# Kernel tuning notes

Measured on AMD Instinct MI355X. Metric: run time of the kernel, lower is better.

## Reference

```python
import jax, jax.numpy as jnp
import numpy as np

D_MODEL = 512
NUM_HEADS = 8


def setup_inputs() -> dict:
    key = jax.random.key(0)
    ks = jax.random.split(key, 12)
    B, S, D = 2, 4096, D_MODEL
    s = 1.0 / np.sqrt(D)
    return {
        "q": jax.random.normal(ks[0], (B, S, D), jnp.float32),
        "k": jax.random.normal(ks[1], (B, S, D), jnp.float32),
        "v": jax.random.normal(ks[2], (B, S, D), jnp.float32),
        "w_q": jax.random.normal(ks[3], (D, D), jnp.float32) * s,
        "b_q": jax.random.normal(ks[4], (D,), jnp.float32) * s,
        "w_k": jax.random.normal(ks[5], (D, D), jnp.float32) * s,
        "b_k": jax.random.normal(ks[6], (D,), jnp.float32) * s,
        "w_v": jax.random.normal(ks[7], (D, D), jnp.float32) * s,
        "b_v": jax.random.normal(ks[8], (D,), jnp.float32) * s,
        "w_o": jax.random.normal(ks[9], (D, D), jnp.float32) * s,
        "b_o": jax.random.normal(ks[10], (D,), jnp.float32) * s,
    }


def _split(x, num_heads):
    B, S, D = x.shape
    return x.reshape(B, S, num_heads, D // num_heads).transpose(0, 2, 1, 3)


def reference(q, k, v, w_q, b_q, w_k, b_k, w_v, b_v, w_o, b_o):
    # Linear projections (torch Linear: x @ W^T + b)
    qp = q @ w_q.T + b_q
    kp = k @ w_k.T + b_k
    vp = v @ w_v.T + b_v
    # split into heads: [B, H, S, d_head]
    qh = _split(qp, NUM_HEADS)
    kh = _split(kp, NUM_HEADS)
    vh = _split(vp, NUM_HEADS)
    d_head = qh.shape[-1]
    # NOTE: original scales by sqrt(d_model of the per-head tensor) == sqrt(d_head)
    score = jnp.einsum("bhqd,bhkd->bhqk", qh, kh) / jnp.sqrt(jnp.float32(d_head))
    attn = jax.nn.softmax(score, axis=-1)  # full [B,H,S,S] materialized, as in source
    out = jnp.einsum("bhqk,bhkd->bhqd", attn, vh)
    # concat heads back to [B, S, D]
    B, H, S, Dh = out.shape
    out = out.transpose(0, 2, 1, 3).reshape(B, S, H * Dh)
    return out @ w_o.T + b_o
```

## Files before the change

### kernel.cpp

```cpp
#include <hip/hip_runtime.h>
#include <math.h>

typedef __bf16 bf16_t;
typedef __bf16 bf16x4_v __attribute__((ext_vector_type(4)));
typedef __bf16 bf16x8_t __attribute__((ext_vector_type(8)));
typedef float f32x4_t __attribute__((ext_vector_type(4)));
typedef short short4_t __attribute__((ext_vector_type(4)));
typedef unsigned uint2_t __attribute__((ext_vector_type(2)));

#define S_LEN 4096
#define DM 512
#define NH 8
#define DH 64
#define MTOT 8192

#define Q_SCALE 0.1803368801111204f

#define REG   4194304
#define WREG  262144
#define W_OFF (3 * REG)
#define CVT_TOTAL (3 * REG + 4 * WREG)
#define QH_OFF CVT_TOTAL

__device__ inline f32x4_t mfma16(bf16x8_t a, bf16x8_t b, f32x4_t c) {
    return __builtin_amdgcn_mfma_f32_16x16x32_bf16(a, b, c, 0, 0, 0);
}

__device__ inline f32x4_t mfma_pv(short4_t a, short4_t b, f32x4_t c) {
    return __builtin_amdgcn_mfma_f32_16x16x16bf16_1k(a, b, c, 0, 0, 0);
}

__device__ inline unsigned pkbf16(float a, float b) {
    unsigned short ra = __builtin_bit_cast(unsigned short, (bf16_t)a);
    unsigned short rb = __builtin_bit_cast(unsigned short, (bf16_t)b);
    return (unsigned)ra | ((unsigned)rb << 16);
}

__device__ inline void async_copy16(const void* g, void* l) {
    __builtin_amdgcn_global_load_lds(
        (const __attribute__((address_space(1))) void*)g,
        (__attribute__((address_space(3))) void*)l, 16, 0, 0);
}

__global__ __launch_bounds__(256) void cvt_all(
    const float* __restrict__ q, const float* __restrict__ k, const float* __restrict__ v,
    const float* __restrict__ wq, const float* __restrict__ wk,
    const float* __restrict__ wv, const float* __restrict__ wo,
    bf16_t* __restrict__ dst)
{
    long gidx = (long)blockIdx.x * 2048 + (long)threadIdx.x * 8;
    const float* src;
    long off = gidx;
    if      (gidx < 1L * REG)          { src = q; }
    else if (gidx < 2L * REG)          { src = k;  off = gidx - 1L * REG; }
    else if (gidx < 3L * REG)          { src = v;  off = gidx - 2L * REG; }
    else if (gidx < W_OFF + 1L * WREG) { src = wq; off = gidx - W_OFF; }
    else if (gidx < W_OFF + 2L * WREG) { src = wk; off = gidx - (W_OFF + 1L * WREG); }
    else if (gidx < W_OFF + 3L * WREG) { src = wv; off = gidx - (W_OFF + 2L * WREG); }
    else                               { src = wo; off = gidx - (W_OFF + 3L * WREG); }
    float4 a = *(const float4*)(src + off);
    float4 b = *(const float4*)(src + off + 4);
    bf16x8_t h;
    h[0] = (bf16_t)a.x; h[1] = (bf16_t)a.y; h[2] = (bf16_t)a.z; h[3] = (bf16_t)a.w;
    h[4] = (bf16_t)b.x; h[5] = (bf16_t)b.y; h[6] = (bf16_t)b.z; h[7] = (bf16_t)b.w;
    *(bf16x8_t*)(dst + gidx) = h;
}

__global__ __launch_bounds__(256) void gemm_qkv(
    const bf16_t* __restrict__ XWb,
    const float* __restrict__ B0, const float* __restrict__ B1, const float* __restrict__ B2,
    bf16_t* __restrict__ dst_base)
{
    const int p = blockIdx.z;
    const bf16_t* __restrict__ X = XWb + (size_t)p * REG;
    const bf16_t* __restrict__ W = XWb + W_OFF + (size_t)p * WREG;
    const float* __restrict__ Bi = (p == 0) ? B0 : ((p == 1) ? B1 : B2);
    bf16_t* __restrict__ dst = dst_base + (size_t)p * REG;

    const int m0 = blockIdx.x * 128;
    const int n0 = blockIdx.y * 128;
    const int tid = threadIdx.x;
    const int lane = tid & 63, wid = tid >> 6;
    const int lm = lane & 15, lg = lane >> 4;
    const int wm = (wid >> 1) * 64, wn = (wid & 1) * 64;

    __shared__ __align__(16) bf16_t As[128 * 64];
    __shared__ __align__(16) bf16_t Bs[128 * 64];

    f32x4_t acc[4][4] = {};

    const int r0 = tid >> 3, c7 = tid & 7;
    const int cA0 = ((lg) ^ (lm & 7)) * 8;
    const int cA1 = ((4 + lg) ^ (lm & 7)) * 8;

    for (int kb = 0; kb < DM / 64; ++kb) {
        const int k0 = kb * 64;
#pragma unroll
        for (int i = 0; i < 4; ++i) {
            int row = i * 32 + r0;
            int ch = c7 ^ (row & 7);
            async_copy16(X + (size_t)(m0 + row) * DM + k0 + ch * 8, (char*)As + (i * 256 + tid) * 16);
            async_copy16(W + (size_t)(n0 + row) * DM + k0 + ch * 8, (char*)Bs + (i * 256 + tid) * 16);
        }
        __syncthreads();
#pragma unroll
        for (int kd = 0; kd < 2; ++kd) {
            const int co = kd ? cA1 : cA0;
            bf16x8_t fa[4], fb[4];
#pragma unroll
            for (int mt = 0; mt < 4; ++mt) {
                fa[mt] = *(const bf16x8_t*)(As + (wm + mt * 16 + lm) * 64 + co);
                fb[mt] = *(const bf16x8_t*)(Bs + (wn + mt * 16 + lm) * 64 + co);
            }
            if (p < 2) {
#pragma unroll
                for (int mt = 0; mt < 4; ++mt)
#pragma unroll
                    for (int nt = 0; nt < 4; ++nt)
                        acc[nt][mt] = mfma16(fb[nt], fa[mt], acc[nt][mt]);
            } else {
#pragma unroll
                for (int mt = 0; mt < 4; ++mt)
#pragma unroll
                    for (int nt = 0; nt < 4; ++nt)
                        acc[mt][nt] = mfma16(fa[mt], fb[nt], acc[mt][nt]);
            }
        }
        __syncthreads();
    }

    if (p == 2) {
#pragma unroll
        for (int nt = 0; nt < 4; ++nt) {
            int col = n0 + wn + nt * 16 + lm;
            float bv = Bi[col];
            int h = (col >> 6) & 7, dc = col & 63;
#pragma unroll
            for (int mt = 0; mt < 4; ++mt) {
                int mrow = m0 + wm + mt * 16 + lg * 4;
                int bb = mrow >> 12, s = mrow & (S_LEN - 1);
                bf16x4_v pk;
#pragma unroll
                for (int r = 0; r < 4; ++r) pk[r] = (bf16_t)(acc[mt][nt][r] + bv);
                *(bf16x4_v*)&dst[(((size_t)(bb * NH + h)) * DH + dc) * S_LEN + s] = pk;
            }
        }
    } else {
        const float scale = (p == 0) ? Q_SCALE : 1.0f;
#pragma unroll
        for (int nt = 0; nt < 4; ++nt) {
            int ncol = n0 + wn + nt * 16 + lg * 4;
            float4 bv4 = *(const float4*)&Bi[ncol];
            int h = (ncol >> 6) & 7, dc = ncol & 63;
#pragma unroll
            for (int mt = 0; mt < 4; ++mt) {
                int m = m0 + wm + mt * 16 + lm;
                int bb = m >> 12, s = m & (S_LEN - 1);
                bf16x4_v pk;
                pk[0] = (bf16_t)((acc[nt][mt][0] + bv4.x) * scale);
                pk[1] = (bf16_t)((acc[nt][mt][1] + bv4.y) * scale);
                pk[2] = (bf16_t)((acc[nt][mt][2] + bv4.z) * scale);
                pk[3] = (bf16_t)((acc[nt][mt][3] + bv4.w) * scale);
                *(bf16x4_v*)&dst[(((size_t)(bb * NH + h)) * S_LEN + s) * DH + dc] = pk;
            }
        }
    }
}

__global__ __launch_bounds__(512, 4) void flash_attn(
    const bf16_t* __restrict__ Qh, const bf16_t* __restrict__ Kh,
    const bf16_t* __restrict__ Vth, bf16_t* __restrict__ O)
{
    const int bh = blockIdx.y;
    const int q0 = blockIdx.x * 128;
    const int tid = threadIdx.x;
    const int lane = tid & 63, wid = tid >> 6;
    const int lm = lane & 15, lg = lane >> 4;
    const int qg = wid & 3;
    const int kvh = wid >> 2;

    const bf16_t* __restrict__ Qb  = Qh  + (size_t)bh * S_LEN * DH;
    const bf16_t* __restrict__ Kb  = Kh  + (size_t)bh * S_LEN * DH;
    const bf16_t* __restrict__ Vtg = Vth + (size_t)bh * S_LEN * DH;

    __shared__ __align__(16) char smem[35328];

    bf16x8_t bQ[2][2];
#pragma unroll
    for (int nt = 0; nt < 2; ++nt)
#pragma unroll
        for (int kd = 0; kd < 2; ++kd)
            bQ[nt][kd] = *(const bf16x8_t*)(Qb + (size_t)(q0 + qg * 32 + nt * 16 + lm) * DH + kd * 32 + lg * 8);

    f32x4_t o_acc[4][2] = {};
    float l_acc[2] = {0.f, 0.f};

    const int srow = tid >> 3;
    const int slch = (tid & 7) ^ (srow & 7);
    char* lK0 = smem + tid * 16;
    char* lK1 = smem + 8192 + tid * 16;
    char* lV0 = smem + 16384 + tid * 16;
    char* lV1 = smem + 24576 + tid * 16;
    const bf16_t* gK = Kb + (size_t)srow * DH + slch * 8;
    const bf16_t* gV = Vtg + (size_t)srow * S_LEN + slch * 8;

    const int cK0 = ((lg) ^ (lm & 7)) * 16;
    const int cK1 = ((4 + lg) ^ (lm & 7)) * 16;
    const char* ksb = smem + kvh * 8192;
    const char* vsb = smem + 16384 + kvh * 8192;

    for (int it = 0; it < S_LEN / 128; ++it) {
        const int kvb = it * 128;
        async_copy16(gK + (size_t)kvb * DH, lK0);
        async_copy16(gK + (size_t)(kvb + 64) * DH, lK1);
        async_copy16(gV + kvb, lV0);
        async_copy16(gV + kvb + 64, lV1);
        __syncthreads();

        unsigned pk[4][2][2];
#pragma unroll
        for (int mt = 0; mt < 4; ++mt) {
            const char* krow = ksb + (mt * 16 + lm) * 128;
            bf16x8_t aK0 = *(const bf16x8_t*)(krow + cK0);
            bf16x8_t aK1 = *(const bf16x8_t*)(krow + cK1);
            f32x4_t s0 = {}, s1 = {};
            s0 = mfma16(aK0, bQ[0][0], s0);
            s0 = mfma16(aK1, bQ[0][1], s0);
            s1 = mfma16(aK0, bQ[1][0], s1);
            s1 = mfma16(aK1, bQ[1][1], s1);
            float e0 = __builtin_amdgcn_exp2f(s0[0]);
            float e1 = __builtin_amdgcn_exp2f(s0[1]);
            float e2 = __builtin_amdgcn_exp2f(s0[2]);
            float e3 = __builtin_amdgcn_exp2f(s0[3]);
            pk[mt][0][0] = pkbf16(e0, e1);
            pk[mt][0][1] = pkbf16(e2, e3);
            l_acc[0] += (e0 + e1) + (e2 + e3);
            float f0 = __builtin_amdgcn_exp2f(s1[0]);
            float f1 = __builtin_amdgcn_exp2f(s1[1]);
            float f2 = __builtin_amdgcn_exp2f(s1[2]);
            float f3 = __builtin_amdgcn_exp2f(s1[3]);
            pk[mt][1][0] = pkbf16(f0, f1);
            pk[mt][1][1] = pkbf16(f2, f3);
            l_acc[1] += (f0 + f1) + (f2 + f3);
        }

#pragma unroll
        for (int mt = 0; mt < 4; ++mt) {
            const char* vrow = vsb + (mt * 16 + lm) * 128;
#pragma unroll
            for (int c = 0; c < 4; ++c) {
                int pc = (c * 2 + (lg >> 1)) ^ (lm & 7);
                short4_t vA = *(const short4_t*)(vrow + pc * 16 + (lg & 1) * 8);
                short4_t bP0 = __builtin_bit_cast(short4_t, (uint2_t){pk[c][0][0], pk[c][0][1]});
                short4_t bP1 = __builtin_bit_cast(short4_t, (uint2_t){pk[c][1][0], pk[c][1][1]});
                o_acc[mt][0] = mfma_pv(vA, bP0, o_acc[mt][0]);
                o_acc[mt][1] = mfma_pv(vA, bP1, o_acc[mt][1]);
            }
        }
        __syncthreads();
    }

#pragma unroll
    for (int nt = 0; nt < 2; ++nt) {
        l_acc[nt] += __shfl_xor(l_acc[nt], 16, 64);
        l_acc[nt] += __shfl_xor(l_acc[nt], 32, 64);
    }

    float* ob = (float*)smem + qg * (32 * 66);
    float* lb = (float*)(smem + 33792);

    if (kvh == 1) {
#pragma unroll
        for (int nt = 0; nt < 2; ++nt) {
#pragma unroll
            for (int mt = 0; mt < 4; ++mt)
#pragma unroll
                for (int r = 0; r < 4; ++r)
                    ob[(nt * 16 + lm) * 66 + mt * 16 + lg * 4 + r] = o_acc[mt][nt][r];
            if (lg == 0) lb[qg * 32 + nt * 16 + lm] = l_acc[nt];
        }
    }
    __syncthreads();
    if (kvh == 0) {
        const int bb = bh >> 3, h = bh & 7;
#pragma unroll
        for (int nt = 0; nt < 2; ++nt) {
            float ltot = l_acc[nt] + lb[qg * 32 + nt * 16 + lm];
            float inv = 1.0f / ltot;
            int q = q0 + qg * 32 + nt * 16 + lm;
            size_t base = ((size_t)(bb * S_LEN + q)) * DM + h * DH;
#pragma unroll
            for (int mt = 0; mt < 4; ++mt) {
                const float* orow = &ob[(nt * 16 + lm) * 66 + mt * 16 + lg * 4];
                bf16x4_v pkd;
#pragma unroll
                for (int r = 0; r < 4; ++r)
                    pkd[r] = (bf16_t)((o_acc[mt][nt][r] + orow[r]) * inv);
                *(bf16x4_v*)&O[base + mt * 16 + lg * 4] = pkd;
            }
        }
    }
}

__global__ __launch_bounds__(256) void gemm_out(
    const bf16_t* __restrict__ A, const bf16_t* __restrict__ W,
    const float* __restrict__ Bi, float* __restrict__ out)
{
    const int m0 = blockIdx.x * 64;
    const int n0 = blockIdx.y * 128;
    const int tid = threadIdx.x;
    const int lane = tid & 63, wid = tid >> 6;
    const int lm = lane & 15, lg = lane >> 4;
    const int wm = (wid >> 1) * 32, wn = (wid & 1) * 64;

    __shared__ __align__(16) bf16_t As[64 * 64];
    __shared__ __align__(16) bf16_t Bs[128 * 64];

    f32x4_t acc[4][2] = {};

    const int r0 = tid >> 3, c7 = tid & 7;
    const int cA0 = ((lg) ^ (lm & 7)) * 8;
    const int cA1 = ((4 + lg) ^ (lm & 7)) * 8;

    for (int kb = 0; kb < DM / 64; ++kb) {
        const int k0 = kb * 64;
#pragma unroll
        for (int i = 0; i < 2; ++i) {
            int idx = i * 256 + tid;
            int row = idx >> 3;
            int ch = (idx & 7) ^ (row & 7);
            async_copy16(A + (size_t)(m0 + row) * DM + k0 + ch * 8, (char*)As + idx * 16);
        }
#pragma unroll
        for (int i = 0; i < 4; ++i) {
            int row = i * 32 + r0;
            int ch = c7 ^ (row & 7);
            async_copy16(W + (size_t)(n0 + row) * DM + k0 + ch * 8, (char*)Bs + (i * 256 + tid) * 16);
        }
        __syncthreads();
#pragma unroll
        for (int kd = 0; kd < 2; ++kd) {
            const int co = kd ? cA1 : cA0;
            bf16x8_t fa[2], fb[4];
#pragma unroll
            for (int mt = 0; mt < 2; ++mt)
                fa[mt] = *(const bf16x8_t*)(As + (wm + mt * 16 + lm) * 64 + co);
#pragma unroll
            for (int nt = 0; nt < 4; ++nt)
                fb[nt] = *(const bf16x8_t*)(Bs + (wn + nt * 16 + lm) * 64 + co);
#pragma unroll
            for (int nt = 0; nt < 4; ++nt)
#pragma unroll
                for (int mt = 0; mt < 2; ++mt)
                    acc[nt][mt] = mfma16(fb[nt], fa[mt], acc[nt][mt]);
        }
        __syncthreads();
    }

#pragma unroll
    for (int nt = 0; nt < 4; ++nt) {
        int ncol = n0 + wn + nt * 16 + lg * 4;
        float4 bv4 = *(const float4*)&Bi[ncol];
#pragma unroll
        for (int mt = 0; mt < 2; ++mt) {
            int m = m0 + wm + mt * 16 + lm;
            float4 ov;
            ov.x = acc[nt][mt][0] + bv4.x;
            ov.y = acc[nt][mt][1] + bv4.y;
            ov.z = acc[nt][mt][2] + bv4.z;
            ov.w = acc[nt][mt][3] + bv4.w;
            *(float4*)&out[(size_t)m * DM + ncol] = ov;
        }
    }
}

extern "C" void kernel_launch(void* const* d_in, const int* in_sizes, int n_in,
                              void* d_out, int out_size, void* d_ws, size_t ws_size,
                              hipStream_t stream)
{
    const float* q  = (const float*)d_in[0];
    const float* k  = (const float*)d_in[1];
    const float* v  = (const float*)d_in[2];
    const float* wq = (const float*)d_in[3];
    const float* bq = (const float*)d_in[4];
    const float* wk = (const float*)d_in[5];
    const float* bk = (const float*)d_in[6];
    const float* wv = (const float*)d_in[7];
    const float* bv = (const float*)d_in[8];
    const float* wo = (const float*)d_in[9];
    const float* bo = (const float*)d_in[10];
    float* out = (float*)d_out;

    bf16_t* ws = (bf16_t*)d_ws;
    bf16_t* XWb = ws;
    bf16_t* Qh  = ws + QH_OFF;
    bf16_t* Kh  = Qh + REG;
    bf16_t* VTh = Kh + REG;
    bf16_t* Ob  = ws;
    bf16_t* Wob = ws + W_OFF + 3 * (size_t)WREG;

    cvt_all<<<CVT_TOTAL / 2048, 256, 0, stream>>>(q, k, v, wq, wk, wv, wo, XWb);

    dim3 g1(MTOT / 128, DM / 128, 3);
    gemm_qkv<<<g1, 256, 0, stream>>>(XWb, bq, bk, bv, Qh);

    dim3 g2(S_LEN / 128, 2 * NH, 1);
    flash_attn<<<g2, 512, 0, stream>>>(Qh, Kh, VTh, Ob);

    dim3 g3(MTOT / 64, DM / 128, 1);
    gemm_out<<<g3, 256, 0, stream>>>(Ob, Wob, bo, out);
}
```

Baseline: 234.9 us.

## Register-prefetch GEMM tiles and use K=32 MFMA for P·V

Result: faster. 229.9 us (-2.1%).

```diff
diff --git a/kernel.cpp b/kernel.cpp
--- a/kernel.cpp
+++ b/kernel.cpp
@@ -5,8 +5,8 @@
 typedef __bf16 bf16x4_v __attribute__((ext_vector_type(4)));
 typedef __bf16 bf16x8_t __attribute__((ext_vector_type(8)));
 typedef float f32x4_t __attribute__((ext_vector_type(4)));
-typedef short short4_t __attribute__((ext_vector_type(4)));
 typedef unsigned uint2_t __attribute__((ext_vector_type(2)));
+typedef unsigned uint4_t __attribute__((ext_vector_type(4)));
 
 #define S_LEN 4096
 #define DM 512
@@ -24,10 +24,6 @@
 
 __device__ inline f32x4_t mfma16(bf16x8_t a, bf16x8_t b, f32x4_t c) {
     return __builtin_amdgcn_mfma_f32_16x16x32_bf16(a, b, c, 0, 0, 0);
-}
-
-__device__ inline f32x4_t mfma_pv(short4_t a, short4_t b, f32x4_t c) {
-    return __builtin_amdgcn_mfma_f32_16x16x16bf16_1k(a, b, c, 0, 0, 0);
 }
 
 __device__ inline unsigned pkbf16(float a, float b) {
@@ -93,16 +89,32 @@
     const int cA0 = ((lg) ^ (lm & 7)) * 8;
     const int cA1 = ((4 + lg) ^ (lm & 7)) * 8;
 
+    int rows[4], chs[4];
+#pragma unroll
+    for (int i = 0; i < 4; ++i) { rows[i] = i * 32 + r0; chs[i] = c7 ^ (rows[i] & 7); }
+
+    uint4_t pA[4], pB[4];
+#pragma unroll
+    for (int i = 0; i < 4; ++i) {
+        pA[i] = *(const uint4_t*)(X + (size_t)(m0 + rows[i]) * DM + chs[i] * 8);
+        pB[i] = *(const uint4_t*)(W + (size_t)(n0 + rows[i]) * DM + chs[i] * 8);
+    }
+#pragma unroll
+    for (int i = 0; i < 4; ++i) {
+        *(uint4_t*)((char*)As + (i * 256 + tid) * 16) = pA[i];
+        *(uint4_t*)((char*)Bs + (i * 256 + tid) * 16) = pB[i];
+    }
+    __syncthreads();
+
     for (int kb = 0; kb < DM / 64; ++kb) {
-        const int k0 = kb * 64;
-#pragma unroll
-        for (int i = 0; i < 4; ++i) {
-            int row = i * 32 + r0;
-            int ch = c7 ^ (row & 7);
-            async_copy16(X + (size_t)(m0 + row) * DM + k0 + ch * 8, (char*)As + (i * 256 + tid) * 16);
-            async_copy16(W + (size_t)(n0 + row) * DM + k0 + ch * 8, (char*)Bs + (i * 256 + tid) * 16);
-        }
-        __syncthreads();
+        if (kb < DM / 64 - 1) {
+            const int k1 = (kb + 1) * 64;
+#pragma unroll
+            for (int i = 0; i < 4; ++i) {
+                pA[i] = *(const uint4_t*)(X + (size_t)(m0 + rows[i]) * DM + k1 + chs[i] * 8);
+                pB[i] = *(const uint4_t*)(W + (size_t)(n0 + rows[i]) * DM + k1 + chs[i] * 8);
+            }
+        }
 #pragma unroll
         for (int kd = 0; kd < 2; ++kd) {
             const int co = kd ? cA1 : cA0;
@@ -126,7 +138,15 @@
                         acc[mt][nt] = mfma16(fa[mt], fb[nt], acc[mt][nt]);
             }
         }
-        __syncthreads();
+        if (kb < DM / 64 - 1) {
+            __syncthreads();
+#pragma unroll
+            for (int i = 0; i < 4; ++i) {
+                *(uint4_t*)((char*)As + (i * 256 + tid) * 16) = pA[i];
+                *(uint4_t*)((char*)Bs + (i * 256 + tid) * 16) = pB[i];
+            }
+            __syncthreads();
+        }
     }
 
     if (p == 2) {
@@ -248,13 +268,17 @@
         for (int mt = 0; mt < 4; ++mt) {
             const char* vrow = vsb + (mt * 16 + lm) * 128;
 #pragma unroll
-            for (int c = 0; c < 4; ++c) {
-                int pc = (c * 2 + (lg >> 1)) ^ (lm & 7);
-                short4_t vA = *(const short4_t*)(vrow + pc * 16 + (lg & 1) * 8);
-                short4_t bP0 = __builtin_bit_cast(short4_t, (uint2_t){pk[c][0][0], pk[c][0][1]});
-                short4_t bP1 = __builtin_bit_cast(short4_t, (uint2_t){pk[c][1][0], pk[c][1][1]});
-                o_acc[mt][0] = mfma_pv(vA, bP0, o_acc[mt][0]);
-                o_acc[mt][1] = mfma_pv(vA, bP1, o_acc[mt][1]);
+            for (int cc = 0; cc < 2; ++cc) {
+                const int ca = 2 * cc, cb = 2 * cc + 1;
+                int pc0 = (ca * 2 + (lg >> 1)) ^ (lm & 7);
+                int pc1 = (cb * 2 + (lg >> 1)) ^ (lm & 7);
+                uint2_t va0 = *(const uint2_t*)(vrow + pc0 * 16 + (lg & 1) * 8);
+                uint2_t va1 = *(const uint2_t*)(vrow + pc1 * 16 + (lg & 1) * 8);
+                bf16x8_t vA = __builtin_bit_cast(bf16x8_t, (uint4_t){va0[0], va0[1], va1[0], va1[1]});
+                bf16x8_t bP0 = __builtin_bit_cast(bf16x8_t, (uint4_t){pk[ca][0][0], pk[ca][0][1], pk[cb][0][0], pk[cb][0][1]});
+                bf16x8_t bP1 = __builtin_bit_cast(bf16x8_t, (uint4_t){pk[ca][1][0], pk[ca][1][1], pk[cb][1][0], pk[cb][1][1]});
+                o_acc[mt][0] = mfma16(vA, bP0, o_acc[mt][0]);
+                o_acc[mt][1] = mfma16(vA, bP1, o_acc[mt][1]);
             }
         }
         __syncthreads();
@@ -322,22 +346,34 @@
     const int cA0 = ((lg) ^ (lm & 7)) * 8;
     const int cA1 = ((4 + lg) ^ (lm & 7)) * 8;
 
+    int arow[2], ach[2], brow[4], bch[4];
+#pragma unroll
+    for (int i = 0; i < 2; ++i) {
+        int idx = i * 256 + tid;
+        arow[i] = idx >> 3; ach[i] = (idx & 7) ^ (arow[i] & 7);
+    }
+#pragma unroll
+    for (int i = 0; i < 4; ++i) { brow[i] = i * 32 + r0; bch[i] = c7 ^ (brow[i] & 7); }
+
+    uint4_t pA[2], pB[4];
+#pragma unroll
+    for (int i = 0; i < 2; ++i) pA[i] = *(const uint4_t*)(A + (size_t)(m0 + arow[i]) * DM + ach[i] * 8);
+#pragma unroll
+    for (int i = 0; i < 4; ++i) pB[i] = *(const uint4_t*)(W + (size_t)(n0 + brow[i]) * DM + bch[i] * 8);
+#pragma unroll
+    for (int i = 0; i < 2; ++i) *(uint4_t*)((char*)As + (i * 256 + tid) * 16) = pA[i];
+#pragma unroll
+    for (int i = 0; i < 4; ++i) *(uint4_t*)((char*)Bs + (i * 256 + tid) * 16) = pB[i];
+    __syncthreads();
+
     for (int kb = 0; kb < DM / 64; ++kb) {
-        const int k0 = kb * 64;
-#pragma unroll
-        for (int i = 0; i < 2; ++i) {
-            int idx = i * 256 + tid;
-            int row = idx >> 3;
-            int ch = (idx & 7) ^ (row & 7);
-            async_copy16(A + (size_t)(m0 + row) * DM + k0 + ch * 8, (char*)As + idx * 16);
-        }
-#pragma unroll
-        for (int i = 0; i < 4; ++i) {
-            int row = i * 32 + r0;
-            int ch = c7 ^ (row & 7);
-            async_copy16(W + (size_t)(n0 + row) * DM + k0 + ch * 8, (char*)Bs + (i * 256 + tid) * 16);
-        }
-        __syncthreads();
+        if (kb < DM / 64 - 1) {
+            const int k1 = (kb + 1) * 64;
+#pragma unroll
+            for (int i = 0; i < 2; ++i) pA[i] = *(const uint4_t*)(A + (size_t)(m0 + arow[i]) * DM + k1 + ach[i] * 8);
+#pragma unroll
+            for (int i = 0; i < 4; ++i) pB[i] = *(const uint4_t*)(W + (size_t)(n0 + brow[i]) * DM + k1 + bch[i] * 8);
+        }
 #pragma unroll
         for (int kd = 0; kd < 2; ++kd) {
             const int co = kd ? cA1 : cA0;
@@ -354,7 +390,14 @@
                 for (int mt = 0; mt < 2; ++mt)
                     acc[nt][mt] = mfma16(fb[nt], fa[mt], acc[nt][mt]);
         }
-        __syncthreads();
+        if (kb < DM / 64 - 1) {
+            __syncthreads();
+#pragma unroll
+            for (int i = 0; i < 2; ++i) *(uint4_t*)((char*)As + (i * 256 + tid) * 16) = pA[i];
+#pragma unroll
+            for (int i = 0; i < 4; ++i) *(uint4_t*)((char*)Bs + (i * 256 + tid) * 16) = pB[i];
+            __syncthreads();
+        }
     }
 
 #pragma unroll
```
